# Optimization experiments

Hardware: AMD Instinct MI355X
Metric: run time of the kernel (lower is better)

Reference implementation:

```python
import jax, jax.numpy as jnp
import numpy as np

MAX_ONSET_DELAY_SAMPLES = 10


def apply_delays(templates, delays):
    # templates: (E, F, L), delays: (E, F) -> shifted templates with zero fill
    E, F, L = templates.shape
    d = jnp.round(jnp.clip(delays, -MAX_ONSET_DELAY_SAMPLES, MAX_ONSET_DELAY_SAMPLES)).astype(jnp.int32)
    idx = jnp.arange(L)                                   # (L,)
    src = idx[None, None, :] - d[:, :, None]              # (E, F, L) source index for torch.roll(shift=d)
    valid = (src >= 0) & (src < L)                        # zero out wrapped-around region
    src_c = jnp.clip(src, 0, L - 1)
    shifted = jnp.take_along_axis(templates, src_c, axis=2)
    return jnp.where(valid, shifted, jnp.zeros((), templates.dtype))


def setup_inputs() -> dict:
    key = jax.random.key(0)
    k1, k2, k3 = jax.random.split(key, 3)
    B, S, F = 64, 32768, 6
    E, L = 16, 80
    x = jax.random.normal(k1, (B, S, F), dtype=jnp.float32)
    templates = jax.random.normal(k2, (E, F, L), dtype=jnp.float32) * 0.1
    onset_delays = jax.random.normal(k3, (E, F), dtype=jnp.float32)
    return {"x": x, "templates": templates, "onset_delays": onset_delays}


def reference(x, templates, onset_delays):
    # x: (B, S, F); templates: (E, F, L); onset_delays: (E, F) -> scores (B, S, E)
    B, S, F = x.shape
    E, _, L = templates.shape
    delayed = apply_delays(templates, onset_delays)       # (E, F, L)
    kern = jnp.flip(delayed, axis=2)                      # torch flips template before conv1d
    pad = (L - 1) // 2
    # Fuse the 96 per-(event,feature) conv1d calls into one conv: sum over features
    # is exactly the input-channel contraction of a dense conv1d (in=F, out=E).
    score = jax.lax.conv_general_dilated(
        jnp.transpose(x, (0, 2, 1)),                      # (B, F, S)
        kern,                                             # (E, F, L) as OIH
        window_strides=(1,),
        padding=[(pad, pad)],
        dimension_numbers=("NCH", "OIH", "NCH"),
    )                                                     # (B, E, S_out)
    S_out = score.shape[2]
    if S_out > S:
        score = score[:, :, :S]
    elif S_out < S:
        score = jnp.pad(score, ((0, 0), (0, 0), (0, S - S_out)))
    return jnp.transpose(score, (0, 2, 1)) / (L * F)      # (B, S, E)
```

## Files before the change

### kernel.cpp

```cpp
#include <hip/hip_runtime.h>

#define BB 64
#define SS 32768
#define FF 6
#define EE 16
#define LL 80
#define KK 480
#define NSL 15
#define TBLK 256
#define NPHI 4
#define WROW 336
#define UPP 166
#define NUNITS 664

typedef _Float16 half8 __attribute__((ext_vector_type(8)));
typedef float f32x4 __attribute__((ext_vector_type(4)));
typedef __fp16 h2 __attribute__((ext_vector_type(2)));

__global__ void prep_kernel(const float* __restrict__ tpl, const float* __restrict__ dly,
                            _Float16* __restrict__ wrev) {
    int n = blockIdx.x * 256 + threadIdx.x;
    if (n >= EE * KK) return;
    int e = n / KK, k = n - e * KK;
    int f = k / LL, r = k - f * LL;
    int m = LL - 1 - r;
    float dl = fminf(fmaxf(dly[e * FF + f], -10.f), 10.f);
    int d = (int)rintf(dl);
    int src = m - d;
    float v = (src >= 0 && src < LL) ? tpl[(e * FF + f) * LL + src] : 0.f;
    wrev[n] = (_Float16)v;
}

template <bool FROM_WS>
__global__ __launch_bounds__(128, 4) void corr_kernel(
    const float* __restrict__ x, const float* __restrict__ tpl,
    const float* __restrict__ dly, const _Float16* __restrict__ wrev,
    float* __restrict__ out) {
    __shared__ alignas(16) _Float16 xs[NPHI][FF][WROW];

    int tid = threadIdx.x;
    int lane = tid & 63;
    int w = tid >> 6;
    int e = lane & 15;
    int g = lane >> 4;

    int b = blockIdx.x >> 7;
    int t0 = (blockIdx.x & 127) << 8;

    const float* xb = x + (size_t)b * (SS * FF);

    f32x4 bqv[NSL];
    if constexpr (FROM_WS) {
        #pragma unroll
        for (int s = 0; s < NSL; s++)
            bqv[s] = *(const f32x4*)&wrev[e * KK + 32 * s + 8 * g];
    } else {
        #pragma unroll
        for (int s = 0; s < NSL; s++) {
            union { f32x4 f4; _Float16 h[8]; } u;
            #pragma unroll
            for (int j = 0; j < 8; j++) {
                int k = 32 * s + 8 * g + j;
                int f = k / LL, r = k - f * LL;
                int m = LL - 1 - r;
                float dl = fminf(fmaxf(dly[e * FF + f], -10.f), 10.f);
                int d = (int)rintf(dl);
                int src = m - d;
                u.h[j] = (_Float16)((src >= 0 && src < LL) ? tpl[(e * FF + f) * LL + src] : 0.f);
            }
            bqv[s] = u.f4;
        }
    }
    #pragma unroll
    for (int s = 0; s < NSL; s++)
        asm volatile("" : "+v"(bqv[s]));

    bool edge = (t0 - 39 < 0) | (t0 + 296 > SS);
    for (int u = tid; u < NUNITS; u += 128) {
        int phi = u / UPP;
        int i2 = (u - phi * UPP) * 2;
        int pos = t0 + phi - 39 + i2;
        float va[12];
        if (!edge) {
            const float* xp = xb + (size_t)pos * FF;
            #pragma unroll
            for (int q = 0; q < 6; q++)
                *(float2*)&va[2 * q] = *(const float2*)&xp[2 * q];
        } else {
            #pragma unroll
            for (int q = 0; q < 2; q++) {
                int p = pos + q;
                bool ok = (p >= 0) && (p < SS);
                #pragma unroll
                for (int f = 0; f < FF; f++)
                    va[q * 6 + f] = ok ? xb[(size_t)p * FF + f] : 0.f;
            }
        }
        #pragma unroll
        for (int f = 0; f < FF; f++) {
            h2 hp = __builtin_amdgcn_cvt_pkrtz(va[f], va[6 + f]);
            *(h2*)&xs[phi][f][i2] = hp;
        }
    }
    __syncthreads();

    #pragma unroll
    for (int phi = 0; phi < NPHI; phi++) {
        const char* xph = (const char*)&xs[phi][0][0];
        #pragma unroll
        for (int tt = 0; tt < 2; tt++) {
            int R = 32 * w + 16 * tt + e;
            f32x4 acc = {0.f, 0.f, 0.f, 0.f};
            #pragma unroll
            for (int s = 0; s < NSL; s++) {
                int k0 = 32 * s + 8 * g;
                int f = (k0 * 205) >> 14;
                int r0 = k0 - 80 * f;
                const char* p = xph + 2 * (f * WROW + 4 * R + r0);
                uint2 lo = *(const uint2*)p;
                uint2 hi = *(const uint2*)(p + 8);
                union { unsigned u[4]; half8 h; } av;
                av.u[0] = lo.x; av.u[1] = lo.y; av.u[2] = hi.x; av.u[3] = hi.y;
                union { f32x4 f4; half8 h; } bv;
                bv.f4 = bqv[s];
                acc = __builtin_amdgcn_mfma_f32_16x16x32_f16(av.h, bv.h, acc, 0, 0, 0);
            }
            #pragma unroll
            for (int j = 0; j < 4; j++) {
                int row = 32 * w + 16 * tt + g * 4 + j;
                int t = t0 + phi + 4 * row;
                float v = acc[j] * (1.0f / 480.0f);
                if (t == SS - 1) v = 0.f;
                out[((size_t)b * SS + t) * EE + e] = v;
            }
        }
    }
}

extern "C" void kernel_launch(void* const* d_in, const int* in_sizes, int n_in,
                              void* d_out, int out_size, void* d_ws, size_t ws_size,
                              hipStream_t stream) {
    const float* x = (const float*)d_in[0];
    const float* tpl = (const float*)d_in[1];
    const float* dly = (const float*)d_in[2];
    float* out = (float*)d_out;

    int grid = BB * (SS / TBLK);
    if (ws_size >= (size_t)(EE * KK * sizeof(_Float16))) {
        _Float16* wrev = (_Float16*)d_ws;
        prep_kernel<<<(EE * KK + 255) / 256, 256, 0, stream>>>(tpl, dly, wrev);
        corr_kernel<true><<<grid, 128, 0, stream>>>(x, tpl, dly, wrev, out);
    } else {
        corr_kernel<false><<<grid, 128, 0, stream>>>(x, tpl, dly, nullptr, out);
    }
}
```

Measured before the change: 73.97 us.

## Pre-convert x to fp16 interleaved layout and stream it into LDS asynchronously

```diff
diff --git a/kernel.cpp b/kernel.cpp
--- a/kernel.cpp
+++ b/kernel.cpp
@@ -8,17 +8,138 @@
 #define KK 480
 #define NSL 15
 #define TBLK 256
-#define NPHI 4
+#define SPLIT 9
+#define NGF (NSL - SPLIT)
+#define SLAB 2048
+#define X16OFF 32768
+
+typedef _Float16 half8 __attribute__((ext_vector_type(8)));
+typedef float f32x4 __attribute__((ext_vector_type(4)));
+typedef float f32x4u __attribute__((ext_vector_type(4), aligned(4)));
+typedef __fp16 h2 __attribute__((ext_vector_type(2)));
+
+__device__ __forceinline__ half8 as_h8(f32x4 v) {
+    union { f32x4 f; half8 h; } u; u.f = v; return u.h;
+}
+__device__ __forceinline__ half8 ldg_h8u(const _Float16* p) {
+    union { f32x4 f; half8 h; } u; u.f = (f32x4)(*(const f32x4u*)p); return u.h;
+}
+
+__global__ __launch_bounds__(256) void prep_all(const float* __restrict__ x,
+                                                const float* __restrict__ tpl,
+                                                const float* __restrict__ dly,
+                                                _Float16* __restrict__ wrev2,
+                                                _Float16* __restrict__ x16) {
+    int tid = threadIdx.x;
+    if (blockIdx.x < 30) {
+        int n = blockIdx.x * 256 + tid;
+        if (n < EE * KK) {
+            int e = n / KK, k = n - e * KK;
+            int r = k / FF, f = k - r * FF;
+            float dl = fminf(fmaxf(dly[e * FF + f], -10.f), 10.f);
+            int d = (int)rintf(dl);
+            int src = LL - 1 - r - d;
+            float v = (src >= 0 && src < LL) ? tpl[(e * FF + f) * LL + src] : 0.f;
+            wrev2[n] = (_Float16)v;
+        }
+    }
+    size_t i = (size_t)blockIdx.x * 256 + tid;
+    const float* xp = x + i * 6;
+    float2 a = *(const float2*)(xp + 0);
+    float2 bq = *(const float2*)(xp + 2);
+    float2 c = *(const float2*)(xp + 4);
+    unsigned u0, u1, u2;
+    { h2 h = __builtin_amdgcn_cvt_pkrtz(a.x, a.y);  u0 = *(unsigned*)&h; }
+    { h2 h = __builtin_amdgcn_cvt_pkrtz(bq.x, bq.y); u1 = *(unsigned*)&h; }
+    { h2 h = __builtin_amdgcn_cvt_pkrtz(c.x, c.y);  u2 = *(unsigned*)&h; }
+    unsigned* dst = (unsigned*)x16 + i * 3;
+    dst[0] = u0; dst[1] = u1; dst[2] = u2;
+}
+
+__global__ __launch_bounds__(256, 3) void corr_new(const _Float16* __restrict__ x16,
+                                                   const _Float16* __restrict__ wrev2,
+                                                   float* __restrict__ out) {
+    __shared__ alignas(16) _Float16 xs[4][SLAB];
+
+    int tid = threadIdx.x, lane = tid & 63, w = tid >> 6;
+    int e = lane & 15, g = lane >> 4;
+    int b = blockIdx.x >> 7;
+    int t0 = (blockIdx.x & 127) << 8;
+
+    f32x4 bqv[NSL];
+    #pragma unroll
+    for (int s = 0; s < NSL; s++)
+        bqv[s] = *(const f32x4*)&wrev2[e * KK + 32 * s + 8 * g];
+    #pragma unroll
+    for (int s = 0; s < NSL; s++)
+        asm volatile("" : "+v"(bqv[s]));
+
+    const _Float16* xw = x16 + ((long)b * SS + t0 + w - 39) * 6;
+
+    #pragma unroll
+    for (int c = 0; c < 4; c++)
+        __builtin_amdgcn_global_load_lds(
+            (const __attribute__((address_space(1))) void*)(xw + 512 * c + 8 * lane),
+            (__attribute__((address_space(3))) void*)&xs[w][512 * c], 16, 0, 0);
+    asm volatile("s_waitcnt vmcnt(0)" ::: "memory");
+    __builtin_amdgcn_sched_barrier(0);
+
+    if (t0 == 0) {
+        int lim = (39 - w) * 6;
+        for (int j = lane; j < lim; j += 64) xs[w][j] = (_Float16)0.f;
+    }
+    bool gsplit = (t0 + TBLK < SS);
+    if (!gsplit) {
+        int lo = (SS - t0 - w + 39) * 6;
+        for (int j = lo + lane; j < SLAB; j += 64) xs[w][j] = (_Float16)0.f;
+    }
+
+    const _Float16* xls = &xs[w][0];
+    #pragma unroll
+    for (int tt = 0; tt < 4; tt++) {
+        int R = tt * 16 + e;
+        int base = 24 * R + 8 * g;
+        f32x4 acc = {0.f, 0.f, 0.f, 0.f};
+
+        half8 gf[NGF];
+        if (gsplit) {
+            #pragma unroll
+            for (int s2 = 0; s2 < NGF; s2++)
+                gf[s2] = ldg_h8u(xw + base + 32 * (SPLIT + s2));
+        }
+        #pragma unroll
+        for (int s = 0; s < SPLIT; s++) {
+            half8 av = *(const half8*)&xls[base + 32 * s];
+            acc = __builtin_amdgcn_mfma_f32_16x16x32_f16(av, as_h8(bqv[s]), acc, 0, 0, 0);
+        }
+        if (gsplit) {
+            #pragma unroll
+            for (int s2 = 0; s2 < NGF; s2++)
+                acc = __builtin_amdgcn_mfma_f32_16x16x32_f16(gf[s2], as_h8(bqv[SPLIT + s2]), acc, 0, 0, 0);
+        } else {
+            #pragma unroll
+            for (int s = SPLIT; s < NSL; s++) {
+                half8 av = *(const half8*)&xls[base + 32 * s];
+                acc = __builtin_amdgcn_mfma_f32_16x16x32_f16(av, as_h8(bqv[s]), acc, 0, 0, 0);
+            }
+        }
+        #pragma unroll
+        for (int j = 0; j < 4; j++) {
+            int row = tt * 16 + g * 4 + j;
+            int t = t0 + w + 4 * row;
+            float v = acc[j] * (1.0f / 480.0f);
+            if (t == SS - 1) v = 0.f;
+            out[((size_t)b * SS + t) * EE + e] = v;
+        }
+    }
+}
+
 #define WROW 336
 #define UPP 166
 #define NUNITS 664
 
-typedef _Float16 half8 __attribute__((ext_vector_type(8)));
-typedef float f32x4 __attribute__((ext_vector_type(4)));
-typedef __fp16 h2 __attribute__((ext_vector_type(2)));
-
-__global__ void prep_kernel(const float* __restrict__ tpl, const float* __restrict__ dly,
-                            _Float16* __restrict__ wrev) {
+__global__ void prep_old(const float* __restrict__ tpl, const float* __restrict__ dly,
+                         _Float16* __restrict__ wrev) {
     int n = blockIdx.x * 256 + threadIdx.x;
     if (n >= EE * KK) return;
     int e = n / KK, k = n - e * KK;
@@ -31,50 +152,21 @@
     wrev[n] = (_Float16)v;
 }
 
-template <bool FROM_WS>
-__global__ __launch_bounds__(128, 4) void corr_kernel(
-    const float* __restrict__ x, const float* __restrict__ tpl,
-    const float* __restrict__ dly, const _Float16* __restrict__ wrev,
-    float* __restrict__ out) {
-    __shared__ alignas(16) _Float16 xs[NPHI][FF][WROW];
-
-    int tid = threadIdx.x;
-    int lane = tid & 63;
-    int w = tid >> 6;
-    int e = lane & 15;
-    int g = lane >> 4;
-
-    int b = blockIdx.x >> 7;
-    int t0 = (blockIdx.x & 127) << 8;
-
+__global__ __launch_bounds__(128, 4) void corr_old(const float* __restrict__ x,
+                                                   const _Float16* __restrict__ wrev,
+                                                   float* __restrict__ out) {
+    __shared__ alignas(16) _Float16 xs[4][FF][WROW];
+    int tid = threadIdx.x, lane = tid & 63, w = tid >> 6;
+    int e = lane & 15, g = lane >> 4;
+    int b = blockIdx.x >> 7, t0 = (blockIdx.x & 127) << 8;
     const float* xb = x + (size_t)b * (SS * FF);
-
     f32x4 bqv[NSL];
-    if constexpr (FROM_WS) {
-        #pragma unroll
-        for (int s = 0; s < NSL; s++)
-            bqv[s] = *(const f32x4*)&wrev[e * KK + 32 * s + 8 * g];
-    } else {
-        #pragma unroll
-        for (int s = 0; s < NSL; s++) {
-            union { f32x4 f4; _Float16 h[8]; } u;
-            #pragma unroll
-            for (int j = 0; j < 8; j++) {
-                int k = 32 * s + 8 * g + j;
-                int f = k / LL, r = k - f * LL;
-                int m = LL - 1 - r;
-                float dl = fminf(fmaxf(dly[e * FF + f], -10.f), 10.f);
-                int d = (int)rintf(dl);
-                int src = m - d;
-                u.h[j] = (_Float16)((src >= 0 && src < LL) ? tpl[(e * FF + f) * LL + src] : 0.f);
-            }
-            bqv[s] = u.f4;
-        }
-    }
+    #pragma unroll
+    for (int s = 0; s < NSL; s++)
+        bqv[s] = *(const f32x4*)&wrev[e * KK + 32 * s + 8 * g];
     #pragma unroll
     for (int s = 0; s < NSL; s++)
         asm volatile("" : "+v"(bqv[s]));
-
     bool edge = (t0 - 39 < 0) | (t0 + 296 > SS);
     for (int u = tid; u < NUNITS; u += 128) {
         int phi = u / UPP;
@@ -84,16 +176,14 @@
         if (!edge) {
             const float* xp = xb + (size_t)pos * FF;
             #pragma unroll
-            for (int q = 0; q < 6; q++)
-                *(float2*)&va[2 * q] = *(const float2*)&xp[2 * q];
+            for (int q = 0; q < 6; q++) *(float2*)&va[2 * q] = *(const float2*)&xp[2 * q];
         } else {
             #pragma unroll
             for (int q = 0; q < 2; q++) {
                 int p = pos + q;
                 bool ok = (p >= 0) && (p < SS);
                 #pragma unroll
-                for (int f = 0; f < FF; f++)
-                    va[q * 6 + f] = ok ? xb[(size_t)p * FF + f] : 0.f;
+                for (int f = 0; f < FF; f++) va[q * 6 + f] = ok ? xb[(size_t)p * FF + f] : 0.f;
             }
         }
         #pragma unroll
@@ -103,9 +193,8 @@
         }
     }
     __syncthreads();
-
-    #pragma unroll
-    for (int phi = 0; phi < NPHI; phi++) {
+    #pragma unroll
+    for (int phi = 0; phi < 4; phi++) {
         const char* xph = (const char*)&xs[phi][0][0];
         #pragma unroll
         for (int tt = 0; tt < 2; tt++) {
@@ -121,9 +210,7 @@
                 uint2 hi = *(const uint2*)(p + 8);
                 union { unsigned u[4]; half8 h; } av;
                 av.u[0] = lo.x; av.u[1] = lo.y; av.u[2] = hi.x; av.u[3] = hi.y;
-                union { f32x4 f4; half8 h; } bv;
-                bv.f4 = bqv[s];
-                acc = __builtin_amdgcn_mfma_f32_16x16x32_f16(av.h, bv.h, acc, 0, 0, 0);
+                acc = __builtin_amdgcn_mfma_f32_16x16x32_f16(av.h, as_h8(bqv[s]), acc, 0, 0, 0);
             }
             #pragma unroll
             for (int j = 0; j < 4; j++) {
@@ -145,12 +232,15 @@
     const float* dly = (const float*)d_in[2];
     float* out = (float*)d_out;
 
-    int grid = BB * (SS / TBLK);
-    if (ws_size >= (size_t)(EE * KK * sizeof(_Float16))) {
+    size_t need = (size_t)X16OFF + (size_t)BB * SS * FF * 2 + 4096;
+    if (ws_size >= need) {
+        _Float16* wrev2 = (_Float16*)d_ws;
+        _Float16* x16 = (_Float16*)((char*)d_ws + X16OFF);
+        prep_all<<<BB * SS / 256, 256, 0, stream>>>(x, tpl, dly, wrev2, x16);
+        corr_new<<<BB * (SS / TBLK), 256, 0, stream>>>(x16, wrev2, out);
+    } else if (ws_size >= (size_t)(EE * KK * sizeof(_Float16))) {
         _Float16* wrev = (_Float16*)d_ws;
-        prep_kernel<<<(EE * KK + 255) / 256, 256, 0, stream>>>(tpl, dly, wrev);
-        corr_kernel<true><<<grid, 128, 0, stream>>>(x, tpl, dly, wrev, out);
-    } else {
-        corr_kernel<false><<<grid, 128, 0, stream>>>(x, tpl, dly, nullptr, out);
-    }
-}
+        prep_old<<<(EE * KK + 255) / 256, 256, 0, stream>>>(tpl, dly, wrev);
+        corr_old<<<BB * (SS / TBLK), 128, 0, stream>>>(x, wrev, out);
+    }
+}
```

Result: slower. 89.07 us (+20.4%).
